# Kernel tuning notes

Hardware: AMD Instinct MI355X
Metric: run time of the kernel (lower is better)

Reference implementation:

```python
import jax, jax.numpy as jnp
import numpy as np

N, E = 20000, 320000
IN_C, HID, OUT_C, HEADS = 512, 32, 40, 8
NEG_SLOPE = 0.2


def setup_inputs() -> dict:
    key = jax.random.key(0)
    ks = jax.random.split(key, 10)
    x = jax.random.normal(ks[0], (N, IN_C), dtype=jnp.float32)
    edge_index = jax.random.randint(ks[1], (2, E), 0, N, dtype=jnp.int64)
    s1 = 1.0 / np.sqrt(IN_C)
    s2 = 1.0 / np.sqrt(HEADS * HID)
    return {
        "x": x,
        "edge_index": edge_index,
        "w1": jax.random.normal(ks[2], (IN_C, HEADS * HID), dtype=jnp.float32) * s1,
        "att_src1": jax.random.normal(ks[3], (HEADS, HID), dtype=jnp.float32) * s2,
        "att_dst1": jax.random.normal(ks[4], (HEADS, HID), dtype=jnp.float32) * s2,
        "b1": jnp.zeros((HEADS * HID,), dtype=jnp.float32),
        "w2": jax.random.normal(ks[5], (HEADS * HID, OUT_C), dtype=jnp.float32) * s2,
        "att_src2": jax.random.normal(ks[6], (1, OUT_C), dtype=jnp.float32) * 0.15,
        "att_dst2": jax.random.normal(ks[7], (1, OUT_C), dtype=jnp.float32) * 0.15,
        "b2": jnp.zeros((OUT_C,), dtype=jnp.float32),
    }


def gat_conv(x, src, dst, w, att_src, att_dst, bias, heads, out_c, concat):
    n = x.shape[0]
    h = (x @ w).reshape(n, heads, out_c)            # [N,H,C]
    a_s = jnp.sum(h * att_src, axis=-1)             # [N,H]
    a_d = jnp.sum(h * att_dst, axis=-1)             # [N,H]
    e = jax.nn.leaky_relu(a_s[src] + a_d[dst], NEG_SLOPE)  # [E,H]
    # segment softmax over destination nodes (self-loops guarantee nonempty)
    m = jax.ops.segment_max(e, dst, num_segments=n)
    e = jnp.exp(e - m[dst])
    z = jax.ops.segment_sum(e, dst, num_segments=n)
    alpha = e / (z[dst] + 1e-16)                    # [E,H]
    msg = alpha[:, :, None] * h[src]                # [E,H,C]
    out = jax.ops.segment_sum(msg, dst, num_segments=n)  # [N,H,C]
    out = out.reshape(n, heads * out_c) if concat else out.mean(axis=1)
    return out + bias


def reference(x, edge_index, w1, att_src1, att_dst1, b1, w2, att_src2, att_dst2, b2):
    n = x.shape[0]
    loops = jnp.arange(n, dtype=edge_index.dtype)
    src = jnp.concatenate([edge_index[0], loops])
    dst = jnp.concatenate([edge_index[1], loops])
    h = gat_conv(x, src, dst, w1, att_src1, att_dst1, b1, HEADS, HID, True)
    h = jax.nn.elu(h)
    out = gat_conv(h, src, dst, w2, att_src2, att_dst2, b2, 1, OUT_C, False)
    return jax.nn.log_softmax(out, axis=1)
```

## Files before the change

### kernel.cpp

```cpp
#include <hip/hip_runtime.h>
#include <hip/hip_bf16.h>
#include <math.h>

#define N_NODES 20000
#define N_EDGES 320000
#define ET (N_EDGES + N_NODES)
#define IN_C 512
#define HEADS 8
#define HID 32
#define HH (HEADS * HID)
#define OUT_C 40
#define NEG_SLOPE 0.2f

typedef __attribute__((ext_vector_type(8))) short short8;
typedef __attribute__((ext_vector_type(4))) float floatx4;

static __device__ __forceinline__ unsigned short f2bf(float f) {
  __hip_bfloat16 h = __float2bfloat16(f);
  return *(unsigned short*)&h;
}
static __device__ __forceinline__ float bf2f_lo(unsigned int u) {
  return __uint_as_float(u << 16);
}
static __device__ __forceinline__ float bf2f_hi(unsigned int u) {
  return __uint_as_float(u & 0xFFFF0000u);
}

#define WCONV_BLOCKS (IN_C * HH / 256)
#define W2CONV_BLOCKS (HH * OUT_C / 256)
#define COUNT_BLOCKS ((ET + 255) / 256)
__global__ __launch_bounds__(256) void prep_kernel(
    const float* __restrict__ w1, const float* __restrict__ w2,
    const int* __restrict__ ei, unsigned short* __restrict__ wbT,
    unsigned short* __restrict__ w2bT, int* __restrict__ deg) {
  if (blockIdx.x < WCONV_BLOCKS) {
    int j = blockIdx.x * 256 + threadIdx.x;
    int k = j >> 8, n = j & 255;
    wbT[(size_t)n * IN_C + k] = f2bf(w1[j]);
  } else if (blockIdx.x < WCONV_BLOCKS + W2CONV_BLOCKS) {
    int j = (blockIdx.x - WCONV_BLOCKS) * 256 + threadIdx.x;
    int k = j / OUT_C, oc = j % OUT_C;
    w2bT[oc * HH + k] = f2bf(w2[j]);
  } else {
    int e = (blockIdx.x - WCONV_BLOCKS - W2CONV_BLOCKS) * 256 + threadIdx.x;
    if (e < ET) {
      int dst = (e < N_EDGES) ? ei[N_EDGES + e] : (e - N_EDGES);
      atomicAdd(&deg[dst], 1);
    }
  }
}

#define BM 64
#define BN 128
#define BK 32
#define APAD 40
#define GY ((N_NODES + BM - 1) / BM)
#define GEMM_BLOCKS (2 * GY)
__global__ __launch_bounds__(256) void gemm1_kernel(
    const float* __restrict__ X, const unsigned short* __restrict__ BT,
    const float* __restrict__ bias, unsigned short* __restrict__ C,
    const int* __restrict__ deg, int* __restrict__ offs, int* __restrict__ cursor) {
  if (blockIdx.x >= GEMM_BLOCKS) {
    __shared__ int wsum[4];
    int t = threadIdx.x;
    int4 buf[20];
    int s = 0;
    if (t < 250) {
      const int4* dp = (const int4*)deg + t * 20;
#pragma unroll
      for (int i = 0; i < 20; i++) {
        buf[i] = dp[i];
        s += buf[i].x + buf[i].y + buf[i].z + buf[i].w;
      }
    }
    int lane = t & 63, w = t >> 6;
    int inc = s;
    for (int o = 1; o < 64; o <<= 1) {
      int u = __shfl_up(inc, o, 64);
      if (lane >= o) inc += u;
    }
    if (lane == 63) wsum[w] = inc;
    __syncthreads();
    int waveOff = 0;
    for (int i = 0; i < w; i++) waveOff += wsum[i];
    int running = waveOff + inc - s;
    if (t < 250) {
      int base = t * 80;
#pragma unroll
      for (int i = 0; i < 20; i++) {
        int4 v = buf[i];
        int4 o;
        o.x = running;
        o.y = o.x + v.x;
        o.z = o.y + v.y;
        o.w = o.z + v.z;
        running = o.w + v.w;
        *(int4*)(offs + base + i * 4) = o;
        *(int4*)(cursor + base + i * 4) = o;
      }
    }
    if (t == 0) offs[N_NODES] = ET;
    return;
  }
  __shared__ unsigned short As[BM][APAD];
  __shared__ unsigned short Bs[BN][APAD];
  const int tid = threadIdx.x;
  const int lane = tid & 63, wave = tid >> 6;
  const int wm = (wave & 1) * 32;
  const int wn = (wave >> 1) * 64;
  const int r16 = lane & 15, q = lane >> 4;
  const int bx = blockIdx.x & 1, by = blockIdx.x >> 1;
  const int rowBase = by * BM;
  const int colBase = bx * BN;
  floatx4 acc[2][4] = {};

  for (int k0 = 0; k0 < IN_C; k0 += BK) {
    {
      int row = tid >> 2, kc = (tid & 3) * 8;
      int arow = rowBase + row;
      float4 v0 = make_float4(0.f, 0.f, 0.f, 0.f), v1 = v0;
      if (arow < N_NODES) {
        const float* p = X + (size_t)arow * IN_C + k0 + kc;
        v0 = *(const float4*)p;
        v1 = *(const float4*)(p + 4);
      }
      unsigned short tmp[8] = {f2bf(v0.x), f2bf(v0.y), f2bf(v0.z), f2bf(v0.w),
                               f2bf(v1.x), f2bf(v1.y), f2bf(v1.z), f2bf(v1.w)};
      *(float4*)&As[row][kc] = *(const float4*)tmp;
    }
#pragma unroll
    for (int i = 0; i < 2; i++) {
      int c = tid + i * 256;
      int row = c >> 2, kc = (c & 3) * 8;
      float4 v = *(const float4*)(BT + (size_t)(colBase + row) * IN_C + k0 + kc);
      *(float4*)&Bs[row][kc] = v;
    }
    __syncthreads();
    short8 afrag[2], bfrag[4];
#pragma unroll
    for (int mt = 0; mt < 2; mt++)
      afrag[mt] = *(const short8*)&As[wm + mt * 16 + r16][q * 8];
#pragma unroll
    for (int nt = 0; nt < 4; nt++)
      bfrag[nt] = *(const short8*)&Bs[wn + nt * 16 + r16][q * 8];
#pragma unroll
    for (int mt = 0; mt < 2; mt++)
#pragma unroll
      for (int nt = 0; nt < 4; nt++)
        acc[mt][nt] = __builtin_amdgcn_mfma_f32_16x16x32_bf16(
            afrag[mt], bfrag[nt], acc[mt][nt], 0, 0, 0);
    __syncthreads();
  }
#pragma unroll
  for (int mt = 0; mt < 2; mt++) {
#pragma unroll
    for (int nt = 0; nt < 4; nt++) {
      int col = colBase + wn + nt * 16 + r16;
      float bb = bias[col];
#pragma unroll
      for (int r = 0; r < 4; r++) {
        int row = rowBase + wm + mt * 16 + q * 4 + r;
        if (row < N_NODES) C[(size_t)row * HH + col] = f2bf(acc[mt][nt][r] + bb);
      }
    }
  }
}

#define FILL_BLOCKS ((ET + 255) / 256)
#define ATTN1_BLOCKS (N_NODES / 4)
__global__ __launch_bounds__(256) void fill_attn1_kernel(
    const int* __restrict__ ei, int* __restrict__ cursor, int* __restrict__ csr,
    const unsigned short* __restrict__ h1b, const float* __restrict__ asrc,
    const float* __restrict__ adst, float* __restrict__ as1, float* __restrict__ ad1) {
  if (blockIdx.x < FILL_BLOCKS) {
    int e = blockIdx.x * 256 + threadIdx.x;
    if (e >= ET) return;
    int src, dst;
    if (e < N_EDGES) { src = ei[e]; dst = ei[N_EDGES + e]; }
    else { src = e - N_EDGES; dst = src; }
    int pos = atomicAdd(&cursor[dst], 1);
    csr[pos] = src;
  } else {
    int wave = threadIdx.x >> 6, lane = threadIdx.x & 63;
    int n = (blockIdx.x - FILL_BLOCKS) * 4 + wave;
    int c4 = lane * 4;
    uint2 raw = *(const uint2*)(h1b + (size_t)n * HH + c4);
    float h0 = bf2f_lo(raw.x), h1 = bf2f_hi(raw.x);
    float h2 = bf2f_lo(raw.y), h3 = bf2f_hi(raw.y);
    float4 sa = *(const float4*)(asrc + c4);
    float4 sd = *(const float4*)(adst + c4);
    float ps = h0 * sa.x + h1 * sa.y + h2 * sa.z + h3 * sa.w;
    float pd = h0 * sd.x + h1 * sd.y + h2 * sd.z + h3 * sd.w;
#pragma unroll
    for (int o = 4; o > 0; o >>= 1) {
      ps += __shfl_down(ps, o, 8);
      pd += __shfl_down(pd, o, 8);
    }
    if ((lane & 7) == 0) {
      as1[n * HEADS + (lane >> 3)] = ps;
      ad1[n * HEADS + (lane >> 3)] = pd;
    }
  }
}

#define NPB 16
#define H2ROW 264
__global__ __launch_bounds__(256) void layer1_fused_kernel(
    const unsigned short* __restrict__ h1b, const float* __restrict__ as1,
    const float* __restrict__ ad1, const int* __restrict__ offs,
    const int* __restrict__ csr, const float* __restrict__ b1,
    const unsigned short* __restrict__ w2bT, const float* __restrict__ b2,
    const float* __restrict__ asrc2, const float* __restrict__ adst2,
    float* __restrict__ h3, float* __restrict__ as2, float* __restrict__ ad2) {
  __shared__ __align__(16) unsigned short h2s[NPB][H2ROW];
  __shared__ float psum[3][NPB], pdsum[3][NPB];
  const int tid = threadIdx.x;
  const int wave = tid >> 6, lane = tid & 63;
  const int r16 = lane & 15, q = lane >> 4;
  const int nodeBase = blockIdx.x * NPB;

  short8 bfrag[8];
  float sa = 0.f, sd = 0.f, b2c = 0.f;
  if (wave < 3) {
    int col = wave * 16 + r16;
    int colc = (col < OUT_C) ? col : 0;
#pragma unroll
    for (int s = 0; s < 8; s++)
      bfrag[s] = *(const short8*)(w2bT + colc * HH + s * 32 + q * 8);
    if (col < OUT_C) { sa = asrc2[col]; sd = adst2[col]; b2c = b2[col]; }
  }

  const int half = lane >> 5, sl = lane & 31;
  const int c8 = sl * 8, head = sl >> 2;
  float4 b0 = *(const float4*)(b1 + c8);
  float4 b4 = *(const float4*)(b1 + c8 + 4);
  for (int i = 0; i < 4; i++) {
    int local = wave * 4 + i;
    int n = nodeBase + local;
    int beg = offs[n], end = offs[n + 1];
    float ad = ad1[n * HEADS + head];
    float acc[8] = {};
    float l = 0.f;
#pragma unroll 2
    for (int k = beg + half; k < end; k += 2) {
      int src = csr[k];
      float e = as1[src * HEADS + head] + ad;
      e = (e > 0.f) ? e : NEG_SLOPE * e;
      float p = __expf(e);
      l += p;
      uint4 raw = *(const uint4*)(h1b + ((unsigned)src << 8) + c8);
      acc[0] = fmaf(p, bf2f_lo(raw.x), acc[0]);
      acc[1] = fmaf(p, bf2f_hi(raw.x), acc[1]);
      acc[2] = fmaf(p, bf2f_lo(raw.y), acc[2]);
      acc[3] = fmaf(p, bf2f_hi(raw.y), acc[3]);
      acc[4] = fmaf(p, bf2f_lo(raw.z), acc[4]);
      acc[5] = fmaf(p, bf2f_hi(raw.z), acc[5]);
      acc[6] = fmaf(p, bf2f_lo(raw.w), acc[6]);
      acc[7] = fmaf(p, bf2f_hi(raw.w), acc[7]);
    }
#pragma unroll
    for (int j = 0; j < 8; j++) acc[j] += __shfl_xor(acc[j], 32, 64);
    l += __shfl_xor(l, 32, 64);
    if (half == 0) {
      float li = 1.f / (l + 1e-16f);
      float v[8];
      v[0] = acc[0] * li + b0.x; v[1] = acc[1] * li + b0.y;
      v[2] = acc[2] * li + b0.z; v[3] = acc[3] * li + b0.w;
      v[4] = acc[4] * li + b4.x; v[5] = acc[5] * li + b4.y;
      v[6] = acc[6] * li + b4.z; v[7] = acc[7] * li + b4.w;
      unsigned short o8[8];
#pragma unroll
      for (int j = 0; j < 8; j++) {
        float e = (v[j] > 0.f) ? v[j] : expm1f(v[j]);
        o8[j] = f2bf(e);
      }
      *(uint4*)&h2s[local][c8] = *(const uint4*)o8;
    }
  }
  __syncthreads();

  if (wave < 3) {
    floatx4 dacc = {};
#pragma unroll
    for (int s = 0; s < 8; s++) {
      short8 afrag = *(const short8*)&h2s[r16][s * 32 + q * 8];
      dacc = __builtin_amdgcn_mfma_f32_16x16x32_bf16(afrag, bfrag[s], dacc, 0, 0, 0);
    }
    int col = wave * 16 + r16;
    float psr[4], pdr[4];
#pragma unroll
    for (int r = 0; r < 4; r++) {
      float val = dacc[r] + b2c;
      if (col < OUT_C)
        h3[(size_t)(nodeBase + q * 4 + r) * OUT_C + col] = val;
      psr[r] = val * sa;
      pdr[r] = val * sd;
    }
#pragma unroll
    for (int o = 8; o > 0; o >>= 1) {
#pragma unroll
      for (int r = 0; r < 4; r++) {
        psr[r] += __shfl_down(psr[r], o, 16);
        pdr[r] += __shfl_down(pdr[r], o, 16);
      }
    }
    if (r16 == 0) {
#pragma unroll
      for (int r = 0; r < 4; r++) {
        psum[wave][q * 4 + r] = psr[r];
        pdsum[wave][q * 4 + r] = pdr[r];
      }
    }
  }
  __syncthreads();
  if (tid < NPB) {
    as2[nodeBase + tid] = psum[0][tid] + psum[1][tid] + psum[2][tid];
    ad2[nodeBase + tid] = pdsum[0][tid] + pdsum[1][tid] + pdsum[2][tid];
  }
}

__global__ __launch_bounds__(256) void agg2_kernel(
    const float* __restrict__ h3, const float* __restrict__ as2,
    const float* __restrict__ ad2, const int* __restrict__ offs,
    const int* __restrict__ csr, const float* __restrict__ b2,
    float* __restrict__ out) {
  int n = blockIdx.x * 4 + (threadIdx.x >> 6);
  int t = threadIdx.x & 63;
  bool act = (t < OUT_C);
  int beg = offs[n], end = offs[n + 1];
  float ad = ad2[n];
  float l = 0.f, acc = 0.f;
#pragma unroll 2
  for (int k = beg; k < end; k++) {
    int src = csr[k];
    float e = as2[src] + ad;
    e = (e > 0.f) ? e : NEG_SLOPE * e;
    float p = __expf(e);
    l += p;
    float hv = act ? h3[(size_t)src * OUT_C + t] : 0.f;
    acc = fmaf(p, hv, acc);
  }
  float v = acc / (l + 1e-16f) + (act ? b2[t] : 0.f);
  float x = act ? v : -INFINITY;
  float mx = x;
  for (int o = 32; o > 0; o >>= 1) mx = fmaxf(mx, __shfl_down(mx, o, 64));
  mx = __shfl(mx, 0, 64);
  float ex = act ? __expf(v - mx) : 0.f;
  float s = ex;
  for (int o = 32; o > 0; o >>= 1) s += __shfl_down(s, o, 64);
  s = __shfl(s, 0, 64);
  if (act) out[(size_t)n * OUT_C + t] = v - mx - logf(s);
}

extern "C" void kernel_launch(void* const* d_in, const int* in_sizes, int n_in,
                              void* d_out, int out_size, void* d_ws, size_t ws_size,
                              hipStream_t stream) {
  const float* x     = (const float*)d_in[0];
  const int*   ei    = (const int*)d_in[1];
  const float* w1    = (const float*)d_in[2];
  const float* asrc1 = (const float*)d_in[3];
  const float* adst1 = (const float*)d_in[4];
  const float* b1    = (const float*)d_in[5];
  const float* w2    = (const float*)d_in[6];
  const float* asrc2 = (const float*)d_in[7];
  const float* adst2 = (const float*)d_in[8];
  const float* b2    = (const float*)d_in[9];
  float* out = (float*)d_out;

  float* fw = (float*)d_ws;
  float* as1   = fw;  fw += (size_t)N_NODES * HEADS;
  float* ad1   = fw;  fw += (size_t)N_NODES * HEADS;
  float* h3    = fw;  fw += (size_t)N_NODES * OUT_C;
  float* as2   = fw;  fw += N_NODES;
  float* ad2   = fw;  fw += N_NODES;
  unsigned short* h1b  = (unsigned short*)fw;  fw += (size_t)N_NODES * HH / 2;
  unsigned short* wbT  = (unsigned short*)fw;  fw += (size_t)IN_C * HH / 2;
  unsigned short* w2bT = (unsigned short*)fw;  fw += (size_t)HH * OUT_C / 2;
  int* deg    = (int*)fw;
  int* offs   = deg + N_NODES;
  int* cursor = offs + N_NODES + 4;
  int* csr    = cursor + N_NODES;

  hipMemsetAsync(deg, 0, N_NODES * sizeof(int), stream);

  prep_kernel<<<WCONV_BLOCKS + W2CONV_BLOCKS + COUNT_BLOCKS, 256, 0, stream>>>(
      w1, w2, ei, wbT, w2bT, deg);
  gemm1_kernel<<<GEMM_BLOCKS + 1, 256, 0, stream>>>(x, wbT, b1, h1b, deg, offs, cursor);
  fill_attn1_kernel<<<FILL_BLOCKS + ATTN1_BLOCKS, 256, 0, stream>>>(
      ei, cursor, csr, h1b, asrc1, adst1, as1, ad1);
  layer1_fused_kernel<<<N_NODES / NPB, 256, 0, stream>>>(
      h1b, as1, ad1, offs, csr, b1, w2bT, b2, asrc2, adst2, h3, as2, ad2);
  agg2_kernel<<<N_NODES / 4, 256, 0, stream>>>(h3, as2, ad2, offs, csr, b2, out);
}
```

Baseline: 235.0 us.

## Merge all stages into one cooperative persistent kernel with grid syncs

Replaces the memset and five separate kernel launches with a single cooperative persistent kernel. It walks virtual blocks in grid-stride loops and separates the stages with grid-wide barriers, and falls back to separate launches if the cooperative launch fails. The goal is to remove launch overhead and the tail gaps between dependent kernels. In exchange it limits parallelism to a fixed grid of at most 1024 resident blocks, runs the scan on one block while the rest wait at a barrier, and adds grid-sync cost. The agg2 loop is also manually unrolled with two independent accumulators.

```diff
diff --git a/kernel.cpp b/kernel.cpp
--- a/kernel.cpp
+++ b/kernel.cpp
@@ -1,6 +1,9 @@
 #include <hip/hip_runtime.h>
+#include <hip/hip_cooperative_groups.h>
 #include <hip/hip_bf16.h>
 #include <math.h>
+
+namespace cg = cooperative_groups;
 
 #define N_NODES 20000
 #define N_EDGES 320000
@@ -12,6 +15,14 @@
 #define OUT_C 40
 #define NEG_SLOPE 0.2f
 
+#define MAX_GRID 1024
+#define GEMM_VB 626
+#define COUNT_VB ((ET + 255) / 256)
+#define FILL_VB ((ET + 255) / 256)
+#define ATTN_VB (N_NODES / 4)
+#define L1_TILES (N_NODES / 16)
+#define AGG2_VB (N_NODES / 4)
+
 typedef __attribute__((ext_vector_type(8))) short short8;
 typedef __attribute__((ext_vector_type(4))) float floatx4;
 
@@ -26,198 +37,185 @@
   return __uint_as_float(u & 0xFFFF0000u);
 }
 
-#define WCONV_BLOCKS (IN_C * HH / 256)
-#define W2CONV_BLOCKS (HH * OUT_C / 256)
-#define COUNT_BLOCKS ((ET + 255) / 256)
-__global__ __launch_bounds__(256) void prep_kernel(
-    const float* __restrict__ w1, const float* __restrict__ w2,
-    const int* __restrict__ ei, unsigned short* __restrict__ wbT,
-    unsigned short* __restrict__ w2bT, int* __restrict__ deg) {
-  if (blockIdx.x < WCONV_BLOCKS) {
-    int j = blockIdx.x * 256 + threadIdx.x;
-    int k = j >> 8, n = j & 255;
-    wbT[(size_t)n * IN_C + k] = f2bf(w1[j]);
-  } else if (blockIdx.x < WCONV_BLOCKS + W2CONV_BLOCKS) {
-    int j = (blockIdx.x - WCONV_BLOCKS) * 256 + threadIdx.x;
-    int k = j / OUT_C, oc = j % OUT_C;
-    w2bT[oc * HH + k] = f2bf(w2[j]);
-  } else {
-    int e = (blockIdx.x - WCONV_BLOCKS - W2CONV_BLOCKS) * 256 + threadIdx.x;
-    if (e < ET) {
-      int dst = (e < N_EDGES) ? ei[N_EDGES + e] : (e - N_EDGES);
-      atomicAdd(&deg[dst], 1);
-    }
-  }
-}
-
-#define BM 64
-#define BN 128
-#define BK 32
-#define APAD 40
-#define GY ((N_NODES + BM - 1) / BM)
-#define GEMM_BLOCKS (2 * GY)
-__global__ __launch_bounds__(256) void gemm1_kernel(
-    const float* __restrict__ X, const unsigned short* __restrict__ BT,
-    const float* __restrict__ bias, unsigned short* __restrict__ C,
-    const int* __restrict__ deg, int* __restrict__ offs, int* __restrict__ cursor) {
-  if (blockIdx.x >= GEMM_BLOCKS) {
-    __shared__ int wsum[4];
-    int t = threadIdx.x;
-    int4 buf[20];
-    int s = 0;
-    if (t < 250) {
-      const int4* dp = (const int4*)deg + t * 20;
-#pragma unroll
-      for (int i = 0; i < 20; i++) {
-        buf[i] = dp[i];
-        s += buf[i].x + buf[i].y + buf[i].z + buf[i].w;
-      }
-    }
-    int lane = t & 63, w = t >> 6;
-    int inc = s;
-    for (int o = 1; o < 64; o <<= 1) {
-      int u = __shfl_up(inc, o, 64);
-      if (lane >= o) inc += u;
-    }
-    if (lane == 63) wsum[w] = inc;
-    __syncthreads();
-    int waveOff = 0;
-    for (int i = 0; i < w; i++) waveOff += wsum[i];
-    int running = waveOff + inc - s;
-    if (t < 250) {
-      int base = t * 80;
-#pragma unroll
-      for (int i = 0; i < 20; i++) {
-        int4 v = buf[i];
-        int4 o;
-        o.x = running;
-        o.y = o.x + v.x;
-        o.z = o.y + v.y;
-        o.w = o.z + v.z;
-        running = o.w + v.w;
-        *(int4*)(offs + base + i * 4) = o;
-        *(int4*)(cursor + base + i * 4) = o;
-      }
-    }
-    if (t == 0) offs[N_NODES] = ET;
-    return;
-  }
-  __shared__ unsigned short As[BM][APAD];
-  __shared__ unsigned short Bs[BN][APAD];
-  const int tid = threadIdx.x;
-  const int lane = tid & 63, wave = tid >> 6;
-  const int wm = (wave & 1) * 32;
-  const int wn = (wave >> 1) * 64;
-  const int r16 = lane & 15, q = lane >> 4;
-  const int bx = blockIdx.x & 1, by = blockIdx.x >> 1;
-  const int rowBase = by * BM;
-  const int colBase = bx * BN;
-  floatx4 acc[2][4] = {};
-
-  for (int k0 = 0; k0 < IN_C; k0 += BK) {
-    {
-      int row = tid >> 2, kc = (tid & 3) * 8;
-      int arow = rowBase + row;
-      float4 v0 = make_float4(0.f, 0.f, 0.f, 0.f), v1 = v0;
-      if (arow < N_NODES) {
-        const float* p = X + (size_t)arow * IN_C + k0 + kc;
-        v0 = *(const float4*)p;
-        v1 = *(const float4*)(p + 4);
-      }
-      unsigned short tmp[8] = {f2bf(v0.x), f2bf(v0.y), f2bf(v0.z), f2bf(v0.w),
-                               f2bf(v1.x), f2bf(v1.y), f2bf(v1.z), f2bf(v1.w)};
-      *(float4*)&As[row][kc] = *(const float4*)tmp;
-    }
-#pragma unroll
-    for (int i = 0; i < 2; i++) {
-      int c = tid + i * 256;
-      int row = c >> 2, kc = (c & 3) * 8;
-      float4 v = *(const float4*)(BT + (size_t)(colBase + row) * IN_C + k0 + kc);
-      *(float4*)&Bs[row][kc] = v;
-    }
-    __syncthreads();
-    short8 afrag[2], bfrag[4];
-#pragma unroll
-    for (int mt = 0; mt < 2; mt++)
-      afrag[mt] = *(const short8*)&As[wm + mt * 16 + r16][q * 8];
-#pragma unroll
-    for (int nt = 0; nt < 4; nt++)
-      bfrag[nt] = *(const short8*)&Bs[wn + nt * 16 + r16][q * 8];
-#pragma unroll
-    for (int mt = 0; mt < 2; mt++)
-#pragma unroll
-      for (int nt = 0; nt < 4; nt++)
-        acc[mt][nt] = __builtin_amdgcn_mfma_f32_16x16x32_bf16(
-            afrag[mt], bfrag[nt], acc[mt][nt], 0, 0, 0);
-    __syncthreads();
-  }
-#pragma unroll
-  for (int mt = 0; mt < 2; mt++) {
-#pragma unroll
-    for (int nt = 0; nt < 4; nt++) {
-      int col = colBase + wn + nt * 16 + r16;
-      float bb = bias[col];
-#pragma unroll
-      for (int r = 0; r < 4; r++) {
-        int row = rowBase + wm + mt * 16 + q * 4 + r;
-        if (row < N_NODES) C[(size_t)row * HH + col] = f2bf(acc[mt][nt][r] + bb);
-      }
-    }
-  }
-}
-
-#define FILL_BLOCKS ((ET + 255) / 256)
-#define ATTN1_BLOCKS (N_NODES / 4)
-__global__ __launch_bounds__(256) void fill_attn1_kernel(
-    const int* __restrict__ ei, int* __restrict__ cursor, int* __restrict__ csr,
-    const unsigned short* __restrict__ h1b, const float* __restrict__ asrc,
-    const float* __restrict__ adst, float* __restrict__ as1, float* __restrict__ ad1) {
-  if (blockIdx.x < FILL_BLOCKS) {
-    int e = blockIdx.x * 256 + threadIdx.x;
-    if (e >= ET) return;
-    int src, dst;
-    if (e < N_EDGES) { src = ei[e]; dst = ei[N_EDGES + e]; }
-    else { src = e - N_EDGES; dst = src; }
-    int pos = atomicAdd(&cursor[dst], 1);
-    csr[pos] = src;
-  } else {
-    int wave = threadIdx.x >> 6, lane = threadIdx.x & 63;
-    int n = (blockIdx.x - FILL_BLOCKS) * 4 + wave;
-    int c4 = lane * 4;
-    uint2 raw = *(const uint2*)(h1b + (size_t)n * HH + c4);
-    float h0 = bf2f_lo(raw.x), h1 = bf2f_hi(raw.x);
-    float h2 = bf2f_lo(raw.y), h3 = bf2f_hi(raw.y);
-    float4 sa = *(const float4*)(asrc + c4);
-    float4 sd = *(const float4*)(adst + c4);
-    float ps = h0 * sa.x + h1 * sa.y + h2 * sa.z + h3 * sa.w;
-    float pd = h0 * sd.x + h1 * sd.y + h2 * sd.z + h3 * sd.w;
-#pragma unroll
-    for (int o = 4; o > 0; o >>= 1) {
-      ps += __shfl_down(ps, o, 8);
-      pd += __shfl_down(pd, o, 8);
-    }
-    if ((lane & 7) == 0) {
-      as1[n * HEADS + (lane >> 3)] = ps;
-      ad1[n * HEADS + (lane >> 3)] = pd;
-    }
-  }
-}
-
-#define NPB 16
-#define H2ROW 264
-__global__ __launch_bounds__(256) void layer1_fused_kernel(
-    const unsigned short* __restrict__ h1b, const float* __restrict__ as1,
-    const float* __restrict__ ad1, const int* __restrict__ offs,
-    const int* __restrict__ csr, const float* __restrict__ b1,
-    const unsigned short* __restrict__ w2bT, const float* __restrict__ b2,
-    const float* __restrict__ asrc2, const float* __restrict__ adst2,
-    float* __restrict__ h3, float* __restrict__ as2, float* __restrict__ ad2) {
-  __shared__ __align__(16) unsigned short h2s[NPB][H2ROW];
-  __shared__ float psum[3][NPB], pdsum[3][NPB];
-  const int tid = threadIdx.x;
+struct Args {
+  const float* x; const int* ei;
+  const float* w1; const float* asrc1; const float* adst1; const float* b1;
+  const float* w2; const float* asrc2; const float* adst2; const float* b2;
+  float* out;
+  float* as1; float* ad1; float* h3; float* as2; float* ad2;
+  unsigned short* h1b; unsigned short* wbT; unsigned short* w2bT;
+  int* deg; int* offs; int* cursor; int* csr;
+};
+
+static __device__ __forceinline__ void phase_prep(const Args& a, int bid, int tid) {
+  for (int gt = bid * 256 + tid; gt < IN_C * HH + HH * OUT_C;
+       gt += gridDim.x * 256) {
+    if (gt < N_NODES) a.deg[gt] = 0;
+    if (gt < IN_C * HH) {
+      int k = gt >> 8, n = gt & 255;
+      a.wbT[(size_t)n * IN_C + k] = f2bf(a.w1[gt]);
+    } else {
+      int j = gt - IN_C * HH;
+      int k = j / OUT_C, oc = j % OUT_C;
+      a.w2bT[oc * HH + k] = f2bf(a.w2[j]);
+    }
+  }
+}
+
+static __device__ void phase_gemm_count(const Args& a, int bid, int tid) {
+  __shared__ unsigned short As[64][40];
+  __shared__ unsigned short Bs[128][40];
+  for (int vb = bid; vb < GEMM_VB + COUNT_VB; vb += gridDim.x) {
+    if (vb < GEMM_VB) {
+      const int lane = tid & 63, wave = tid >> 6;
+      const int wm = (wave & 1) * 32;
+      const int wn = (wave >> 1) * 64;
+      const int r16 = lane & 15, q = lane >> 4;
+      const int rowBase = (vb >> 1) * 64;
+      const int colBase = (vb & 1) * 128;
+      floatx4 acc[2][4] = {};
+      for (int k0 = 0; k0 < IN_C; k0 += 32) {
+        {
+          int row = tid >> 2, kc = (tid & 3) * 8;
+          int arow = rowBase + row;
+          float4 v0 = make_float4(0.f, 0.f, 0.f, 0.f), v1 = v0;
+          if (arow < N_NODES) {
+            const float* p = a.x + (size_t)arow * IN_C + k0 + kc;
+            v0 = *(const float4*)p;
+            v1 = *(const float4*)(p + 4);
+          }
+          unsigned short tmp[8] = {f2bf(v0.x), f2bf(v0.y), f2bf(v0.z), f2bf(v0.w),
+                                   f2bf(v1.x), f2bf(v1.y), f2bf(v1.z), f2bf(v1.w)};
+          *(float4*)&As[row][kc] = *(const float4*)tmp;
+        }
+#pragma unroll
+        for (int i = 0; i < 2; i++) {
+          int c = tid + i * 256;
+          int row = c >> 2, kc = (c & 3) * 8;
+          float4 v = *(const float4*)(a.wbT + (size_t)(colBase + row) * IN_C + k0 + kc);
+          *(float4*)&Bs[row][kc] = v;
+        }
+        __syncthreads();
+        short8 afrag[2], bfrag[4];
+#pragma unroll
+        for (int mt = 0; mt < 2; mt++)
+          afrag[mt] = *(const short8*)&As[wm + mt * 16 + r16][q * 8];
+#pragma unroll
+        for (int nt = 0; nt < 4; nt++)
+          bfrag[nt] = *(const short8*)&Bs[wn + nt * 16 + r16][q * 8];
+#pragma unroll
+        for (int mt = 0; mt < 2; mt++)
+#pragma unroll
+          for (int nt = 0; nt < 4; nt++)
+            acc[mt][nt] = __builtin_amdgcn_mfma_f32_16x16x32_bf16(
+                afrag[mt], bfrag[nt], acc[mt][nt], 0, 0, 0);
+        __syncthreads();
+      }
+#pragma unroll
+      for (int mt = 0; mt < 2; mt++) {
+#pragma unroll
+        for (int nt = 0; nt < 4; nt++) {
+          int col = colBase + wn + nt * 16 + r16;
+          float bb = a.b1[col];
+#pragma unroll
+          for (int r = 0; r < 4; r++) {
+            int row = rowBase + wm + mt * 16 + q * 4 + r;
+            if (row < N_NODES)
+              a.h1b[(size_t)row * HH + col] = f2bf(acc[mt][nt][r] + bb);
+          }
+        }
+      }
+    } else {
+      int e = (vb - GEMM_VB) * 256 + tid;
+      if (e < ET) {
+        int dst = (e < N_EDGES) ? a.ei[N_EDGES + e] : (e - N_EDGES);
+        atomicAdd(&a.deg[dst], 1);
+      }
+    }
+  }
+}
+
+static __device__ void phase_scan(const Args& a, int t) {
+  __shared__ int wsum[4];
+  int4 buf[20];
+  int s = 0;
+  if (t < 250) {
+    const int4* dp = (const int4*)a.deg + t * 20;
+#pragma unroll
+    for (int i = 0; i < 20; i++) {
+      buf[i] = dp[i];
+      s += buf[i].x + buf[i].y + buf[i].z + buf[i].w;
+    }
+  }
+  int lane = t & 63, w = t >> 6;
+  int inc = s;
+  for (int o = 1; o < 64; o <<= 1) {
+    int u = __shfl_up(inc, o, 64);
+    if (lane >= o) inc += u;
+  }
+  if (lane == 63) wsum[w] = inc;
+  __syncthreads();
+  int waveOff = 0;
+  for (int i = 0; i < w; i++) waveOff += wsum[i];
+  int running = waveOff + inc - s;
+  if (t < 250) {
+    int base = t * 80;
+#pragma unroll
+    for (int i = 0; i < 20; i++) {
+      int4 v = buf[i];
+      int4 o;
+      o.x = running;
+      o.y = o.x + v.x;
+      o.z = o.y + v.y;
+      o.w = o.z + v.z;
+      running = o.w + v.w;
+      *(int4*)(a.offs + base + i * 4) = o;
+      *(int4*)(a.cursor + base + i * 4) = o;
+    }
+  }
+  if (t == 0) a.offs[N_NODES] = ET;
+}
+
+static __device__ void phase_fill_attn(const Args& a, int bid, int tid) {
+  const int wave = tid >> 6, lane = tid & 63;
+  for (int vb = bid; vb < FILL_VB + ATTN_VB; vb += gridDim.x) {
+    if (vb < FILL_VB) {
+      int e = vb * 256 + tid;
+      if (e < ET) {
+        int src, dst;
+        if (e < N_EDGES) { src = a.ei[e]; dst = a.ei[N_EDGES + e]; }
+        else { src = e - N_EDGES; dst = src; }
+        int pos = atomicAdd(&a.cursor[dst], 1);
+        a.csr[pos] = src;
+      }
+    } else {
+      int n = (vb - FILL_VB) * 4 + wave;
+      int c4 = lane * 4;
+      uint2 raw = *(const uint2*)(a.h1b + (size_t)n * HH + c4);
+      float h0 = bf2f_lo(raw.x), h1 = bf2f_hi(raw.x);
+      float h2 = bf2f_lo(raw.y), h3 = bf2f_hi(raw.y);
+      float4 sa = *(const float4*)(a.asrc1 + c4);
+      float4 sd = *(const float4*)(a.adst1 + c4);
+      float ps = h0 * sa.x + h1 * sa.y + h2 * sa.z + h3 * sa.w;
+      float pd = h0 * sd.x + h1 * sd.y + h2 * sd.z + h3 * sd.w;
+#pragma unroll
+      for (int o = 4; o > 0; o >>= 1) {
+        ps += __shfl_down(ps, o, 8);
+        pd += __shfl_down(pd, o, 8);
+      }
+      if ((lane & 7) == 0) {
+        a.as1[n * HEADS + (lane >> 3)] = ps;
+        a.ad1[n * HEADS + (lane >> 3)] = pd;
+      }
+    }
+  }
+}
+
+static __device__ void phase_layer1(const Args& a, int bid, int tid) {
+  __shared__ __align__(16) unsigned short h2s[16][264];
+  __shared__ float psum[3][16], pdsum[3][16];
   const int wave = tid >> 6, lane = tid & 63;
   const int r16 = lane & 15, q = lane >> 4;
-  const int nodeBase = blockIdx.x * NPB;
 
   short8 bfrag[8];
   float sa = 0.f, sd = 0.f, b2c = 0.f;
@@ -226,169 +224,217 @@
     int colc = (col < OUT_C) ? col : 0;
 #pragma unroll
     for (int s = 0; s < 8; s++)
-      bfrag[s] = *(const short8*)(w2bT + colc * HH + s * 32 + q * 8);
-    if (col < OUT_C) { sa = asrc2[col]; sd = adst2[col]; b2c = b2[col]; }
-  }
-
+      bfrag[s] = *(const short8*)(a.w2bT + colc * HH + s * 32 + q * 8);
+    if (col < OUT_C) { sa = a.asrc2[col]; sd = a.adst2[col]; b2c = a.b2[col]; }
+  }
   const int half = lane >> 5, sl = lane & 31;
   const int c8 = sl * 8, head = sl >> 2;
-  float4 b0 = *(const float4*)(b1 + c8);
-  float4 b4 = *(const float4*)(b1 + c8 + 4);
-  for (int i = 0; i < 4; i++) {
-    int local = wave * 4 + i;
-    int n = nodeBase + local;
-    int beg = offs[n], end = offs[n + 1];
-    float ad = ad1[n * HEADS + head];
-    float acc[8] = {};
-    float l = 0.f;
+  float4 b0 = *(const float4*)(a.b1 + c8);
+  float4 b4 = *(const float4*)(a.b1 + c8 + 4);
+
+  for (int tile = bid; tile < L1_TILES; tile += gridDim.x) {
+    const int nodeBase = tile * 16;
+    for (int i = 0; i < 4; i++) {
+      int local = wave * 4 + i;
+      int n = nodeBase + local;
+      int beg = a.offs[n], end = a.offs[n + 1];
+      float ad = a.ad1[n * HEADS + head];
+      float acc[8] = {};
+      float l = 0.f;
 #pragma unroll 2
-    for (int k = beg + half; k < end; k += 2) {
-      int src = csr[k];
-      float e = as1[src * HEADS + head] + ad;
-      e = (e > 0.f) ? e : NEG_SLOPE * e;
-      float p = __expf(e);
-      l += p;
-      uint4 raw = *(const uint4*)(h1b + ((unsigned)src << 8) + c8);
-      acc[0] = fmaf(p, bf2f_lo(raw.x), acc[0]);
-      acc[1] = fmaf(p, bf2f_hi(raw.x), acc[1]);
-      acc[2] = fmaf(p, bf2f_lo(raw.y), acc[2]);
-      acc[3] = fmaf(p, bf2f_hi(raw.y), acc[3]);
-      acc[4] = fmaf(p, bf2f_lo(raw.z), acc[4]);
-      acc[5] = fmaf(p, bf2f_hi(raw.z), acc[5]);
-      acc[6] = fmaf(p, bf2f_lo(raw.w), acc[6]);
-      acc[7] = fmaf(p, bf2f_hi(raw.w), acc[7]);
-    }
-#pragma unroll
-    for (int j = 0; j < 8; j++) acc[j] += __shfl_xor(acc[j], 32, 64);
-    l += __shfl_xor(l, 32, 64);
-    if (half == 0) {
-      float li = 1.f / (l + 1e-16f);
-      float v[8];
-      v[0] = acc[0] * li + b0.x; v[1] = acc[1] * li + b0.y;
-      v[2] = acc[2] * li + b0.z; v[3] = acc[3] * li + b0.w;
-      v[4] = acc[4] * li + b4.x; v[5] = acc[5] * li + b4.y;
-      v[6] = acc[6] * li + b4.z; v[7] = acc[7] * li + b4.w;
-      unsigned short o8[8];
-#pragma unroll
-      for (int j = 0; j < 8; j++) {
-        float e = (v[j] > 0.f) ? v[j] : expm1f(v[j]);
-        o8[j] = f2bf(e);
-      }
-      *(uint4*)&h2s[local][c8] = *(const uint4*)o8;
-    }
-  }
-  __syncthreads();
-
-  if (wave < 3) {
-    floatx4 dacc = {};
-#pragma unroll
-    for (int s = 0; s < 8; s++) {
-      short8 afrag = *(const short8*)&h2s[r16][s * 32 + q * 8];
-      dacc = __builtin_amdgcn_mfma_f32_16x16x32_bf16(afrag, bfrag[s], dacc, 0, 0, 0);
-    }
-    int col = wave * 16 + r16;
-    float psr[4], pdr[4];
-#pragma unroll
-    for (int r = 0; r < 4; r++) {
-      float val = dacc[r] + b2c;
-      if (col < OUT_C)
-        h3[(size_t)(nodeBase + q * 4 + r) * OUT_C + col] = val;
-      psr[r] = val * sa;
-      pdr[r] = val * sd;
-    }
-#pragma unroll
-    for (int o = 8; o > 0; o >>= 1) {
+      for (int k = beg + half; k < end; k += 2) {
+        int src = a.csr[k];
+        float e = a.as1[src * HEADS + head] + ad;
+        e = (e > 0.f) ? e : NEG_SLOPE * e;
+        float p = __expf(e);
+        l += p;
+        uint4 raw = *(const uint4*)(a.h1b + ((unsigned)src << 8) + c8);
+        acc[0] = fmaf(p, bf2f_lo(raw.x), acc[0]);
+        acc[1] = fmaf(p, bf2f_hi(raw.x), acc[1]);
+        acc[2] = fmaf(p, bf2f_lo(raw.y), acc[2]);
+        acc[3] = fmaf(p, bf2f_hi(raw.y), acc[3]);
+        acc[4] = fmaf(p, bf2f_lo(raw.z), acc[4]);
+        acc[5] = fmaf(p, bf2f_hi(raw.z), acc[5]);
+        acc[6] = fmaf(p, bf2f_lo(raw.w), acc[6]);
+        acc[7] = fmaf(p, bf2f_hi(raw.w), acc[7]);
+      }
+#pragma unroll
+      for (int j = 0; j < 8; j++) acc[j] += __shfl_xor(acc[j], 32, 64);
+      l += __shfl_xor(l, 32, 64);
+      if (half == 0) {
+        float li = 1.f / (l + 1e-16f);
+        float v[8];
+        v[0] = acc[0] * li + b0.x; v[1] = acc[1] * li + b0.y;
+        v[2] = acc[2] * li + b0.z; v[3] = acc[3] * li + b0.w;
+        v[4] = acc[4] * li + b4.x; v[5] = acc[5] * li + b4.y;
+        v[6] = acc[6] * li + b4.z; v[7] = acc[7] * li + b4.w;
+        unsigned short o8[8];
+#pragma unroll
+        for (int j = 0; j < 8; j++) {
+          float e = (v[j] > 0.f) ? v[j] : expm1f(v[j]);
+          o8[j] = f2bf(e);
+        }
+        *(uint4*)&h2s[local][c8] = *(const uint4*)o8;
+      }
+    }
+    __syncthreads();
+    if (wave < 3) {
+      floatx4 dacc = {};
+#pragma unroll
+      for (int s = 0; s < 8; s++) {
+        short8 afrag = *(const short8*)&h2s[r16][s * 32 + q * 8];
+        dacc = __builtin_amdgcn_mfma_f32_16x16x32_bf16(afrag, bfrag[s], dacc, 0, 0, 0);
+      }
+      int col = wave * 16 + r16;
+      float psr[4], pdr[4];
 #pragma unroll
       for (int r = 0; r < 4; r++) {
-        psr[r] += __shfl_down(psr[r], o, 16);
-        pdr[r] += __shfl_down(pdr[r], o, 16);
-      }
-    }
-    if (r16 == 0) {
-#pragma unroll
-      for (int r = 0; r < 4; r++) {
-        psum[wave][q * 4 + r] = psr[r];
-        pdsum[wave][q * 4 + r] = pdr[r];
-      }
-    }
-  }
-  __syncthreads();
-  if (tid < NPB) {
-    as2[nodeBase + tid] = psum[0][tid] + psum[1][tid] + psum[2][tid];
-    ad2[nodeBase + tid] = pdsum[0][tid] + pdsum[1][tid] + pdsum[2][tid];
-  }
-}
-
-__global__ __launch_bounds__(256) void agg2_kernel(
-    const float* __restrict__ h3, const float* __restrict__ as2,
-    const float* __restrict__ ad2, const int* __restrict__ offs,
-    const int* __restrict__ csr, const float* __restrict__ b2,
-    float* __restrict__ out) {
-  int n = blockIdx.x * 4 + (threadIdx.x >> 6);
-  int t = threadIdx.x & 63;
+        float val = dacc[r] + b2c;
+        if (col < OUT_C)
+          a.h3[(size_t)(nodeBase + q * 4 + r) * OUT_C + col] = val;
+        psr[r] = val * sa;
+        pdr[r] = val * sd;
+      }
+#pragma unroll
+      for (int o = 8; o > 0; o >>= 1) {
+#pragma unroll
+        for (int r = 0; r < 4; r++) {
+          psr[r] += __shfl_down(psr[r], o, 16);
+          pdr[r] += __shfl_down(pdr[r], o, 16);
+        }
+      }
+      if (r16 == 0) {
+#pragma unroll
+        for (int r = 0; r < 4; r++) {
+          psum[wave][q * 4 + r] = psr[r];
+          pdsum[wave][q * 4 + r] = pdr[r];
+        }
+      }
+    }
+    __syncthreads();
+    if (tid < 16) {
+      a.as2[nodeBase + tid] = psum[0][tid] + psum[1][tid] + psum[2][tid];
+      a.ad2[nodeBase + tid] = pdsum[0][tid] + pdsum[1][tid] + pdsum[2][tid];
+    }
+    __syncthreads();
+  }
+}
+
+static __device__ void phase_agg2(const Args& a, int bid, int tid) {
+  const int wave = tid >> 6, t = tid & 63;
   bool act = (t < OUT_C);
-  int beg = offs[n], end = offs[n + 1];
-  float ad = ad2[n];
-  float l = 0.f, acc = 0.f;
-#pragma unroll 2
-  for (int k = beg; k < end; k++) {
-    int src = csr[k];
-    float e = as2[src] + ad;
-    e = (e > 0.f) ? e : NEG_SLOPE * e;
-    float p = __expf(e);
-    l += p;
-    float hv = act ? h3[(size_t)src * OUT_C + t] : 0.f;
-    acc = fmaf(p, hv, acc);
-  }
-  float v = acc / (l + 1e-16f) + (act ? b2[t] : 0.f);
-  float x = act ? v : -INFINITY;
-  float mx = x;
-  for (int o = 32; o > 0; o >>= 1) mx = fmaxf(mx, __shfl_down(mx, o, 64));
-  mx = __shfl(mx, 0, 64);
-  float ex = act ? __expf(v - mx) : 0.f;
-  float s = ex;
-  for (int o = 32; o > 0; o >>= 1) s += __shfl_down(s, o, 64);
-  s = __shfl(s, 0, 64);
-  if (act) out[(size_t)n * OUT_C + t] = v - mx - logf(s);
-}
+  for (int vb = bid; vb < AGG2_VB; vb += gridDim.x) {
+    int n = vb * 4 + wave;
+    int beg = a.offs[n], end = a.offs[n + 1];
+    float ad = a.ad2[n];
+    float l0 = 0.f, l1 = 0.f, a0 = 0.f, a1 = 0.f;
+    int k = beg;
+    for (; k + 1 < end; k += 2) {
+      int s0 = a.csr[k], s1 = a.csr[k + 1];
+      float e0 = a.as2[s0] + ad, e1 = a.as2[s1] + ad;
+      e0 = (e0 > 0.f) ? e0 : NEG_SLOPE * e0;
+      e1 = (e1 > 0.f) ? e1 : NEG_SLOPE * e1;
+      float p0 = __expf(e0), p1 = __expf(e1);
+      l0 += p0; l1 += p1;
+      float h0 = act ? a.h3[(size_t)s0 * OUT_C + t] : 0.f;
+      float h1 = act ? a.h3[(size_t)s1 * OUT_C + t] : 0.f;
+      a0 = fmaf(p0, h0, a0);
+      a1 = fmaf(p1, h1, a1);
+    }
+    if (k < end) {
+      int s0 = a.csr[k];
+      float e0 = a.as2[s0] + ad;
+      e0 = (e0 > 0.f) ? e0 : NEG_SLOPE * e0;
+      float p0 = __expf(e0);
+      l0 += p0;
+      float h0 = act ? a.h3[(size_t)s0 * OUT_C + t] : 0.f;
+      a0 = fmaf(p0, h0, a0);
+    }
+    float l = l0 + l1, acc = a0 + a1;
+    float v = acc / (l + 1e-16f) + (act ? a.b2[t] : 0.f);
+    float x = act ? v : -INFINITY;
+    float mx = x;
+    for (int o = 32; o > 0; o >>= 1) mx = fmaxf(mx, __shfl_down(mx, o, 64));
+    mx = __shfl(mx, 0, 64);
+    float ex = act ? __expf(v - mx) : 0.f;
+    float s = ex;
+    for (int o = 32; o > 0; o >>= 1) s += __shfl_down(s, o, 64);
+    s = __shfl(s, 0, 64);
+    if (act) a.out[(size_t)n * OUT_C + t] = v - mx - logf(s);
+  }
+}
+
+__global__ __launch_bounds__(256, 4) void mega_kernel(Args a) {
+  cg::grid_group g = cg::this_grid();
+  const int bid = blockIdx.x, tid = threadIdx.x;
+  phase_prep(a, bid, tid);
+  g.sync();
+  phase_gemm_count(a, bid, tid);
+  g.sync();
+  if (bid == 0) phase_scan(a, tid);
+  g.sync();
+  phase_fill_attn(a, bid, tid);
+  g.sync();
+  phase_layer1(a, bid, tid);
+  g.sync();
+  phase_agg2(a, bid, tid);
+}
+
+__global__ __launch_bounds__(256, 4) void k_prep(Args a) { phase_prep(a, blockIdx.x, threadIdx.x); }
+__global__ __launch_bounds__(256, 4) void k_gemm(Args a) { phase_gemm_count(a, blockIdx.x, threadIdx.x); }
+__global__ __launch_bounds__(256) void k_scan(Args a) { phase_scan(a, threadIdx.x); }
+__global__ __launch_bounds__(256, 4) void k_fill(Args a) { phase_fill_attn(a, blockIdx.x, threadIdx.x); }
+__global__ __launch_bounds__(256, 4) void k_layer1(Args a) { phase_layer1(a, blockIdx.x, threadIdx.x); }
+__global__ __launch_bounds__(256, 4) void k_agg2(Args a) { phase_agg2(a, blockIdx.x, threadIdx.x); }
 
 extern "C" void kernel_launch(void* const* d_in, const int* in_sizes, int n_in,
                               void* d_out, int out_size, void* d_ws, size_t ws_size,
                               hipStream_t stream) {
-  const float* x     = (const float*)d_in[0];
-  const int*   ei    = (const int*)d_in[1];
-  const float* w1    = (const float*)d_in[2];
-  const float* asrc1 = (const float*)d_in[3];
-  const float* adst1 = (const float*)d_in[4];
-  const float* b1    = (const float*)d_in[5];
-  const float* w2    = (const float*)d_in[6];
-  const float* asrc2 = (const float*)d_in[7];
-  const float* adst2 = (const float*)d_in[8];
-  const float* b2    = (const float*)d_in[9];
-  float* out = (float*)d_out;
+  Args a;
+  a.x     = (const float*)d_in[0];
+  a.ei    = (const int*)d_in[1];
+  a.w1    = (const float*)d_in[2];
+  a.asrc1 = (const float*)d_in[3];
+  a.adst1 = (const float*)d_in[4];
+  a.b1    = (const float*)d_in[5];
+  a.w2    = (const float*)d_in[6];
+  a.asrc2 = (const float*)d_in[7];
+  a.adst2 = (const float*)d_in[8];
+  a.b2    = (const float*)d_in[9];
+  a.out   = (float*)d_out;
 
   float* fw = (float*)d_ws;
-  float* as1   = fw;  fw += (size_t)N_NODES * HEADS;
-  float* ad1   = fw;  fw += (size_t)N_NODES * HEADS;
-  float* h3    = fw;  fw += (size_t)N_NODES * OUT_C;
-  float* as2   = fw;  fw += N_NODES;
-  float* ad2   = fw;  fw += N_NODES;
-  unsigned short* h1b  = (unsigned short*)fw;  fw += (size_t)N_NODES * HH / 2;
-  unsigned short* wbT  = (unsigned short*)fw;  fw += (size_t)IN_C * HH / 2;
-  unsigned short* w2bT = (unsigned short*)fw;  fw += (size_t)HH * OUT_C / 2;
-  int* deg    = (int*)fw;
-  int* offs   = deg + N_NODES;
-  int* cursor = offs + N_NODES + 4;
-  int* csr    = cursor + N_NODES;
-
-  hipMemsetAsync(deg, 0, N_NODES * sizeof(int), stream);
-
-  prep_kernel<<<WCONV_BLOCKS + W2CONV_BLOCKS + COUNT_BLOCKS, 256, 0, stream>>>(
-      w1, w2, ei, wbT, w2bT, deg);
-  gemm1_kernel<<<GEMM_BLOCKS + 1, 256, 0, stream>>>(x, wbT, b1, h1b, deg, offs, cursor);
-  fill_attn1_kernel<<<FILL_BLOCKS + ATTN1_BLOCKS, 256, 0, stream>>>(
-      ei, cursor, csr, h1b, asrc1, adst1, as1, ad1);
-  layer1_fused_kernel<<<N_NODES / NPB, 256, 0, stream>>>(
-      h1b, as1, ad1, offs, csr, b1, w2bT, b2, asrc2, adst2, h3, as2, ad2);
-  agg2_kernel<<<N_NODES / 4, 256, 0, stream>>>(h3, as2, ad2, offs, csr, b2, out);
-}
+  a.as1 = fw;  fw += (size_t)N_NODES * HEADS;
+  a.ad1 = fw;  fw += (size_t)N_NODES * HEADS;
+  a.h3  = fw;  fw += (size_t)N_NODES * OUT_C;
+  a.as2 = fw;  fw += N_NODES;
+  a.ad2 = fw;  fw += N_NODES;
+  a.h1b  = (unsigned short*)fw;  fw += (size_t)N_NODES * HH / 2;
+  a.wbT  = (unsigned short*)fw;  fw += (size_t)IN_C * HH / 2;
+  a.w2bT = (unsigned short*)fw;  fw += (size_t)HH * OUT_C / 2;
+  a.deg    = (int*)fw;
+  a.offs   = a.deg + N_NODES;
+  a.cursor = a.offs + N_NODES + 4;
+  a.csr    = a.cursor + N_NODES;
+
+  int perCU = 0;
+  hipError_t qerr = hipOccupancyMaxActiveBlocksPerMultiprocessor(
+      &perCU, (const void*)mega_kernel, 256, 0);
+  int grid = MAX_GRID;
+  if (qerr == hipSuccess && perCU > 0) {
+    int cap = perCU * 256;
+    if (cap < grid) grid = cap;
+  }
+
+  void* params[] = {(void*)&a};
+  hipError_t st = hipLaunchCooperativeKernel(
+      (const void*)mega_kernel, dim3(grid), dim3(256), params, 0, stream);
+  if (st != hipSuccess) {
+    k_prep<<<MAX_GRID, 256, 0, stream>>>(a);
+    k_gemm<<<MAX_GRID, 256, 0, stream>>>(a);
+    k_scan<<<1, 256, 0, stream>>>(a);
+    k_fill<<<MAX_GRID, 256, 0, stream>>>(a);
+    k_layer1<<<MAX_GRID, 256, 0, stream>>>(a);
+    k_agg2<<<MAX_GRID, 256, 0, stream>>>(a);
+  }
+}
```

Result: slower. 597.4 us (+154.3%).
